# Performance work log

Hardware: AMD Instinct MI355X
Metric: run time of the kernel (lower is better)

The kernel has to match this reference:

```python
import jax, jax.numpy as jnp
import numpy as np

NUM_HEADS = 16
HIDDEN = 1024
HEAD_DIM = HIDDEN // NUM_HEADS


def setup_inputs() -> dict:
    key = jax.random.key(0)
    ks = jax.random.split(key, 9)
    B, S = 2, 2048
    s = 1.0 / np.sqrt(HIDDEN)
    return {
        "x": jax.random.normal(ks[0], (B, S, HIDDEN), dtype=jnp.float32),
        "Wq": jax.random.normal(ks[1], (HIDDEN, HIDDEN), dtype=jnp.float32) * s,
        "bq": jnp.zeros((HIDDEN,), dtype=jnp.float32),
        "Wk": jax.random.normal(ks[2], (HIDDEN, HIDDEN), dtype=jnp.float32) * s,
        "bk": jnp.zeros((HIDDEN,), dtype=jnp.float32),
        "Wv": jax.random.normal(ks[3], (HIDDEN, HIDDEN), dtype=jnp.float32) * s,
        "bv": jnp.zeros((HIDDEN,), dtype=jnp.float32),
        "Wo": jax.random.normal(ks[4], (HIDDEN, HIDDEN), dtype=jnp.float32) * s,
        "bo": jnp.zeros((HIDDEN,), dtype=jnp.float32),
    }


def reference(x, Wq, bq, Wk, bk, Wv, bv, Wo, bo):
    B, S, H = x.shape
    # project and split heads: [B, S, H] -> [B, nh, S, hd]
    def split_heads(t):
        return t.reshape(B, S, NUM_HEADS, HEAD_DIM).transpose(0, 2, 1, 3)

    q = split_heads(x @ Wq + bq)
    k = split_heads(x @ Wk + bk)
    v = split_heads(x @ Wv + bv)

    scores = jnp.einsum("bhqd,bhkd->bhqk", q, k) / jnp.sqrt(
        jnp.asarray(HEAD_DIM, dtype=x.dtype))
    probs = jax.nn.softmax(scores, axis=-1)
    # attn_drop_rate = 0.0 -> dropout is identity
    ctx = jnp.einsum("bhqk,bhkd->bhqd", probs, v)
    ctx = ctx.transpose(0, 2, 1, 3).reshape(B, S, H)
    out = ctx @ Wo + bo
    return out
```

## Files before the change

kernel.cpp:

```cpp
#include <hip/hip_runtime.h>

#define NHEADS 16
#define HDIM   64
#define SEQL   2048
#define HID    1024
#define NB     2
#define MT     4096

#define QSCALE 0.18033688011112042f
#define RESCALE_THR 6.0f

typedef float        f4_t   __attribute__((ext_vector_type(4)));
typedef float        f32x16 __attribute__((ext_vector_type(16)));
typedef unsigned int u32x4  __attribute__((ext_vector_type(4)));
typedef __bf16       bf16x8 __attribute__((ext_vector_type(8)));

typedef const __attribute__((address_space(1))) unsigned int* gas_ptr;
typedef __attribute__((address_space(3))) unsigned int*       las_ptr;

__device__ __forceinline__ void gload16(const void* g, void* l){
  __builtin_amdgcn_global_load_lds((gas_ptr)g, (las_ptr)l, 16, 0, 0);
}
__device__ __forceinline__ unsigned int pkbf(float a, float b){
  unsigned short lo = __builtin_bit_cast(unsigned short, (__bf16)a);
  unsigned short hi = __builtin_bit_cast(unsigned short, (__bf16)b);
  return (unsigned)lo | ((unsigned)hi << 16);
}
__device__ __forceinline__ unsigned short f2bf(float f){
  return __builtin_bit_cast(unsigned short, (__bf16)f);
}
__device__ __forceinline__ u32x4 ld16(const unsigned short* p){
  return *reinterpret_cast<const u32x4*>(p);
}
__device__ __forceinline__ f4_t mfma_bf16(u32x4 a, u32x4 b, f4_t c){
  return __builtin_amdgcn_mfma_f32_16x16x32_bf16(
      __builtin_bit_cast(bf16x8, a), __builtin_bit_cast(bf16x8, b), c, 0, 0, 0);
}
__device__ __forceinline__ f32x16 mfma32(u32x4 a, u32x4 b, f32x16 c){
  return __builtin_amdgcn_mfma_f32_32x32x16_bf16(
      __builtin_bit_cast(bf16x8, a), __builtin_bit_cast(bf16x8, b), c, 0, 0, 0);
}

#if __has_builtin(__builtin_amdgcn_permlane32_swap)
typedef unsigned int u32x2 __attribute__((ext_vector_type(2)));
__device__ __forceinline__ void plswap(unsigned int &a, unsigned int &b){
  u32x2 r = __builtin_amdgcn_permlane32_swap(a, b, false, false);
  a = r[0]; b = r[1];
}
#else
__device__ __forceinline__ void plswap(unsigned int &a, unsigned int &b){
  unsigned int as = (unsigned int)__shfl_xor((int)a, 32);
  unsigned int bs = (unsigned int)__shfl_xor((int)b, 32);
  bool hi = (threadIdx.x & 32) != 0;
  unsigned int na = hi ? bs : a;
  unsigned int nb = hi ? b  : as;
  a = na; b = nb;
}
#endif

__global__ __launch_bounds__(256) void xcast(const float* __restrict__ x,
                                             unsigned short* __restrict__ xb){
  int gid = blockIdx.x * 256 + threadIdx.x;
  float4 a = reinterpret_cast<const float4*>(x)[gid * 2];
  float4 b = reinterpret_cast<const float4*>(x)[gid * 2 + 1];
  u32x4 o;
  o[0] = pkbf(a.x, a.y);
  o[1] = pkbf(a.z, a.w);
  o[2] = pkbf(b.x, b.y);
  o[3] = pkbf(b.z, b.w);
  *reinterpret_cast<u32x4*>(&xb[gid * 8]) = o;
}

__global__ void prep_w(const float* __restrict__ Wq, const float* __restrict__ Wk,
                       const float* __restrict__ Wv, const float* __restrict__ Wo,
                       unsigned short* __restrict__ wqT, unsigned short* __restrict__ wkT,
                       unsigned short* __restrict__ wvT, unsigned short* __restrict__ woT){
  __shared__ float t[32][33];
  int z = blockIdx.z;
  const float* W = (z==0)?Wq:(z==1)?Wk:(z==2)?Wv:Wo;
  unsigned short* WT = (z==0)?wqT:(z==1)?wkT:(z==2)?wvT:woT;
  float sc = (z==0) ? QSCALE : 1.0f;
  int k0 = blockIdx.x*32, n0 = blockIdx.y*32;
  int tx = threadIdx.x, ty = threadIdx.y;
  #pragma unroll
  for (int ii=0; ii<4; ii++)
    t[ty+ii*8][tx] = W[(k0+ty+ii*8)*HID + n0+tx];
  __syncthreads();
  #pragma unroll
  for (int ii=0; ii<4; ii++)
    WT[(n0+ty+ii*8)*HID + k0+tx] = f2bf(t[tx][ty+ii*8] * sc);
}

__global__ __launch_bounds__(256) void qkv_gemm(
    const unsigned short* __restrict__ xb,
    const unsigned short* __restrict__ wqT, const unsigned short* __restrict__ wkT,
    const unsigned short* __restrict__ wvT,
    const float* __restrict__ bq, const float* __restrict__ bk, const float* __restrict__ bv,
    unsigned short* __restrict__ qo, unsigned short* __restrict__ ko,
    unsigned short* __restrict__ vto){
  __shared__ unsigned short As[128*32];
  __shared__ unsigned short Bs[128*32];
  const int z = blockIdx.z;
  const unsigned short* wT = (z==0)?wqT:(z==1)?wkT:wvT;
  const float* bias = (z==0)?bq:(z==1)?bk:bv;
  const float bscale = (z==0) ? QSCALE : 1.0f;
  const int m0 = blockIdx.x * 128;
  const int n0 = blockIdx.y * 128;
  const int tid = threadIdx.x;
  const int lane = tid & 63, w = tid >> 6;
  const int l15 = lane & 15, lg = lane >> 4;
  const int wr = (w >> 1) * 64, wc = (w & 1) * 64;
  const int srow = w*16 + (lane >> 2);
  const int skc  = (lane & 3) * 8;

  f4_t acc[4][4];
  f4_t z4 = {0.f, 0.f, 0.f, 0.f};
  #pragma unroll
  for (int i=0;i<4;i++)
    #pragma unroll
    for (int j=0;j<4;j++) acc[i][j] = z4;

  for (int kt = 0; kt < HID; kt += 32) {
    __syncthreads();
    #pragma unroll
    for (int c = 0; c < 2; c++) {
      int row = c*64 + srow;
      gload16(&xb[(m0+row)*HID + kt + skc], (char*)As + c*4096 + w*1024);
      gload16(&wT[(n0+row)*HID + kt + skc], (char*)Bs + c*4096 + w*1024);
    }
    __syncthreads();
    u32x4 a[4], b[4];
    #pragma unroll
    for (int i=0;i<4;i++) a[i] = ld16(&As[(wr + i*16 + l15)*32 + lg*8]);
    #pragma unroll
    for (int j=0;j<4;j++) b[j] = ld16(&Bs[(wc + j*16 + l15)*32 + lg*8]);
    #pragma unroll
    for (int i=0;i<4;i++)
      #pragma unroll
      for (int j=0;j<4;j++)
        acc[i][j] = mfma_bf16(a[i], b[j], acc[i][j]);
  }
  if (z == 2) {
    #pragma unroll
    for (int i=0;i<4;i++){
      int mrow = m0 + wr + i*16 + lg*4;
      int b_ = mrow >> 11, s = mrow & 2047;
      #pragma unroll
      for (int j=0;j<4;j++){
        int n = n0 + wc + j*16 + l15;
        float bs = bias[n];
        int h = n >> 6, d = n & 63;
        unsigned int lo = pkbf(acc[i][j][0]+bs, acc[i][j][1]+bs);
        unsigned int hi = pkbf(acc[i][j][2]+bs, acc[i][j][3]+bs);
        unsigned long long v8 = (unsigned long long)lo | ((unsigned long long)hi << 32);
        *reinterpret_cast<unsigned long long*>(
            vto + (((b_*NHEADS + h)*HDIM + d)*SEQL + s)) = v8;
      }
    }
  } else {
    unsigned short* outp = (z==0) ? qo : ko;
    #pragma unroll
    for (int i=0;i<4;i++){
      int mrow = m0 + wr + i*16 + lg*4;
      #pragma unroll
      for (int j=0;j<4;j++){
        int n = n0 + wc + j*16 + l15;
        float bs = bias[n] * bscale;
        int h = n >> 6, d = n & 63;
        #pragma unroll
        for (int r=0;r<4;r++){
          int m = mrow + r;
          int b_ = m >> 11, s = m & 2047;
          outp[(((b_*NHEADS + h)*SEQL) + s)*HDIM + d] = f2bf(acc[i][j][r] + bs);
        }
      }
    }
  }
}

__global__ __launch_bounds__(256) void flash(
    const unsigned short* __restrict__ q,
    const unsigned short* __restrict__ k,
    const unsigned short* __restrict__ vT,
    unsigned short* __restrict__ ctx){
  __shared__ unsigned short Ks[2][4096];
  __shared__ unsigned short Vs[2][4096];
  const int bh = blockIdx.y;
  const int b_ = bh >> 4, h = bh & 15;
  const int tid = threadIdx.x;
  const int w = tid >> 6, lane = tid & 63;
  const int l31 = lane & 31, hi = lane >> 5;
  const int q0 = blockIdx.x*128 + w*32;
  const unsigned short* qb = q + (bh*SEQL + q0)*HDIM;
  const unsigned short* kp = k + bh*SEQL*HDIM;
  const unsigned short* vp = vT + bh*HDIM*SEQL;

  const int sr = w*16 + (lane >> 3);
  const int scol = ((lane & 7) ^ (sr & 7)) * 8;
  const int ldst = w*2048;

  u32x4 qf[4];
  #pragma unroll
  for (int c=0;c<4;c++)
    qf[c] = ld16(&qb[l31*HDIM + c*16 + hi*8]);

  float mr = -1e30f, lsum = 0.f;
  f32x16 oacc[2];
  f32x16 z16 = {0.f,0.f,0.f,0.f,0.f,0.f,0.f,0.f,0.f,0.f,0.f,0.f,0.f,0.f,0.f,0.f};
  oacc[0] = z16; oacc[1] = z16;

  auto stage = [&](int buf, int kb){
    const unsigned short* gk = kp + (kb + sr)*HDIM + scol;
    gload16(gk,          (char*)Ks[buf] + ldst);
    gload16(gk + 8*HDIM, (char*)Ks[buf] + ldst + 1024);
    const unsigned short* gv = vp + sr*SEQL + kb + scol;
    gload16(gv,          (char*)Vs[buf] + ldst);
    gload16(gv + 8*SEQL, (char*)Vs[buf] + ldst + 1024);
  };

  int cur = 0;
  stage(0, 0);
  __syncthreads();

  const int rs = (l31 & 7) << 4;

  for (int kb = 0; kb < SEQL; kb += 64) {
    if (kb + 64 < SEQL) stage(cur^1, kb + 64);
    const char* kbase = (const char*)Ks[cur];
    const char* vbase = (const char*)Vs[cur];

    f32x16 sacc[2];
    __builtin_amdgcn_s_setprio(1);
    #pragma unroll
    for (int t=0;t<2;t++){
      const char* rowb = kbase + (t*32 + l31)*128;
      #pragma unroll
      for (int c=0;c<4;c++){
        u32x4 kf = *reinterpret_cast<const u32x4*>(rowb + ((c*32 + hi*16) ^ rs));
        sacc[t] = (c==0) ? mfma32(kf, qf[0], z16) : mfma32(kf, qf[c], sacc[t]);
      }
    }
    __builtin_amdgcn_s_setprio(0);

    float mx[16];
    #pragma unroll
    for (int r=0;r<16;r++) mx[r] = fmaxf(sacc[0][r], sacc[1][r]);
    #pragma unroll
    for (int r=0;r<8;r++) mx[r] = fmaxf(mx[r], mx[r+8]);
    #pragma unroll
    for (int r=0;r<4;r++) mx[r] = fmaxf(mx[r], mx[r+4]);
    float vm = fmaxf(fmaxf(mx[0], mx[1]), fmaxf(mx[2], mx[3]));
    vm = fmaxf(vm, __shfl_xor(vm, 32));
    if (!__all(vm - mr <= RESCALE_THR)) {
      float mnew = fmaxf(mr, vm);
      float scl = exp2f(mr - mnew);
      mr = mnew;
      lsum *= scl;
      oacc[0] *= scl;
      oacc[1] *= scl;
    }
    float sm[16];
    #pragma unroll
    for (int t=0;t<2;t++)
      #pragma unroll
      for (int r=0;r<16;r++) sacc[t][r] = exp2f(sacc[t][r] - mr);
    #pragma unroll
    for (int r=0;r<16;r++) sm[r] = sacc[0][r] + sacc[1][r];
    #pragma unroll
    for (int r=0;r<8;r++) sm[r] += sm[r+8];
    #pragma unroll
    for (int r=0;r<4;r++) sm[r] += sm[r+4];
    float ps = (sm[0] + sm[1]) + (sm[2] + sm[3]);
    ps += __shfl_xor(ps, 32);
    lsum += ps;

    u32x4 pa[4];
    #pragma unroll
    for (int t=0;t<2;t++)
      #pragma unroll
      for (int hf=0;hf<2;hf++){
        unsigned int c1 = pkbf(sacc[t][hf*8+0], sacc[t][hf*8+1]);
        unsigned int c2 = pkbf(sacc[t][hf*8+2], sacc[t][hf*8+3]);
        unsigned int c3 = pkbf(sacc[t][hf*8+4], sacc[t][hf*8+5]);
        unsigned int c4 = pkbf(sacc[t][hf*8+6], sacc[t][hf*8+7]);
        plswap(c1, c3);
        plswap(c2, c4);
        u32x4 f; f[0]=c1; f[1]=c2; f[2]=c3; f[3]=c4;
        pa[t*2+hf] = f;
      }

    __builtin_amdgcn_s_setprio(1);
    #pragma unroll
    for (int dt=0;dt<2;dt++){
      const char* rowb = vbase + (dt*32 + l31)*128;
      #pragma unroll
      for (int ks=0;ks<4;ks++){
        u32x4 vf = *reinterpret_cast<const u32x4*>(rowb + ((ks*32 + hi*16) ^ rs));
        oacc[dt] = mfma32(vf, pa[ks], oacc[dt]);
      }
    }
    __builtin_amdgcn_s_setprio(0);
    __syncthreads();
    cur ^= 1;
  }

  float inv = 1.0f / lsum;
  unsigned short* cb = ctx + (b_*SEQL + q0 + l31)*HID + h*HDIM;
  #pragma unroll
  for (int dt=0;dt<2;dt++){
    #pragma unroll
    for (int kq=0;kq<4;kq++){
      unsigned int lo = pkbf(oacc[dt][kq*4+0]*inv, oacc[dt][kq*4+1]*inv);
      unsigned int hi2 = pkbf(oacc[dt][kq*4+2]*inv, oacc[dt][kq*4+3]*inv);
      unsigned long long v8 = (unsigned long long)lo | ((unsigned long long)hi2 << 32);
      *reinterpret_cast<unsigned long long*>(cb + dt*32 + kq*8 + hi*4) = v8;
    }
  }
}

__global__ __launch_bounds__(256) void out_gemm(
    const unsigned short* __restrict__ cb,
    const unsigned short* __restrict__ woT,
    const float* __restrict__ bo,
    float* __restrict__ out){
  __shared__ unsigned short As[128*32];
  __shared__ unsigned short Bs[128*32];
  const int m0 = blockIdx.x * 128;
  const int n0 = blockIdx.y * 128;
  const int tid = threadIdx.x;
  const int lane = tid & 63, w = tid >> 6;
  const int l15 = lane & 15, lg = lane >> 4;
  const int wr = (w >> 1) * 64, wc = (w & 1) * 64;
  const int srow = w*16 + (lane >> 2);
  const int skc  = (lane & 3) * 8;

  f4_t acc[4][4];
  f4_t z4 = {0.f,0.f,0.f,0.f};
  #pragma unroll
  for (int i=0;i<4;i++)
    #pragma unroll
    for (int j=0;j<4;j++) acc[i][j] = z4;

  for (int kt = 0; kt < HID; kt += 32) {
    __syncthreads();
    #pragma unroll
    for (int c = 0; c < 2; c++) {
      int row = c*64 + srow;
      gload16(&cb[(m0+row)*HID + kt + skc],  (char*)As + c*4096 + w*1024);
      gload16(&woT[(n0+row)*HID + kt + skc], (char*)Bs + c*4096 + w*1024);
    }
    __syncthreads();
    u32x4 a[4], b[4];
    #pragma unroll
    for (int i=0;i<4;i++) a[i] = ld16(&As[(wr + i*16 + l15)*32 + lg*8]);
    #pragma unroll
    for (int j=0;j<4;j++) b[j] = ld16(&Bs[(wc + j*16 + l15)*32 + lg*8]);
    #pragma unroll
    for (int i=0;i<4;i++)
      #pragma unroll
      for (int j=0;j<4;j++)
        acc[i][j] = mfma_bf16(a[i], b[j], acc[i][j]);
  }
  #pragma unroll
  for (int i=0;i<4;i++){
    int mrow = m0 + wr + i*16 + lg*4;
    #pragma unroll
    for (int j=0;j<4;j++){
      int n = n0 + wc + j*16 + l15;
      float bs = bo[n];
      #pragma unroll
      for (int r=0;r<4;r++)
        out[(mrow + r)*HID + n] = acc[i][j][r] + bs;
    }
  }
}

extern "C" void kernel_launch(void* const* d_in, const int* in_sizes, int n_in,
                              void* d_out, int out_size, void* d_ws, size_t ws_size,
                              hipStream_t stream){
  const float* x  = (const float*)d_in[0];
  const float* Wq = (const float*)d_in[1];
  const float* bq = (const float*)d_in[2];
  const float* Wk = (const float*)d_in[3];
  const float* bk = (const float*)d_in[4];
  const float* Wv = (const float*)d_in[5];
  const float* bv = (const float*)d_in[6];
  const float* Wo = (const float*)d_in[7];
  const float* bo = (const float*)d_in[8];
  float* out = (float*)d_out;

  char* ws = (char*)d_ws;
  size_t off = 0;
  auto alloc = [&](size_t bytes) -> void* {
    void* p = ws + off;
    off += (bytes + 255) & ~(size_t)255;
    return p;
  };
  unsigned short* xb   = (unsigned short*)alloc((size_t)MT*HID*2);
  unsigned short* wqT  = (unsigned short*)alloc((size_t)HID*HID*2);
  unsigned short* wkT  = (unsigned short*)alloc((size_t)HID*HID*2);
  unsigned short* wvT  = (unsigned short*)alloc((size_t)HID*HID*2);
  unsigned short* woT  = (unsigned short*)alloc((size_t)HID*HID*2);
  unsigned short* q_ws = (unsigned short*)alloc((size_t)MT*HID*2);
  unsigned short* k_ws = (unsigned short*)alloc((size_t)MT*HID*2);
  unsigned short* vT_ws= (unsigned short*)alloc((size_t)MT*HID*2);
  unsigned short* c_ws = (unsigned short*)alloc((size_t)MT*HID*2);

  prep_w<<<dim3(32,32,4), dim3(32,8), 0, stream>>>(Wq,Wk,Wv,Wo, wqT,wkT,wvT,woT);
  xcast<<<dim3(2048), dim3(256), 0, stream>>>(x, xb);
  qkv_gemm<<<dim3(32,8,3), dim3(256), 0, stream>>>(xb, wqT,wkT,wvT, bq,bk,bv,
                                                   q_ws, k_ws, vT_ws);
  flash<<<dim3(16,32), dim3(256), 0, stream>>>(q_ws, k_ws, vT_ws, c_ws);
  out_gemm<<<dim3(32,8), dim3(256), 0, stream>>>(c_ws, woT, bo, out);
}
```

Baseline: 170.2 us.

## Split flash attention over key range and merge partials in a combine kernel

The flash kernel now splits the key sequence across blockIdx.z (flash-decoding style). Each split writes fp32 partial outputs plus running max and sum, and a new combine kernel rescales and merges them into the bf16 context. The aim is to raise the grid from 512 to 1024 blocks so the many CUs are better filled. The row sum is now computed with an MFMA against a ones vector, the row max uses a 3-input max tree, and launch bounds request 4 blocks per CU. The cost is extra fp32 partial traffic and an additional kernel launch, with a fallback to one split if the workspace is too small.

```diff
diff --git a/kernel.cpp b/kernel.cpp
--- a/kernel.cpp
+++ b/kernel.cpp
@@ -39,6 +39,9 @@
 __device__ __forceinline__ f32x16 mfma32(u32x4 a, u32x4 b, f32x16 c){
   return __builtin_amdgcn_mfma_f32_32x32x16_bf16(
       __builtin_bit_cast(bf16x8, a), __builtin_bit_cast(bf16x8, b), c, 0, 0, 0);
+}
+__device__ __forceinline__ float max3f(float a, float b, float c){
+  return fmaxf(fmaxf(a, b), c);
 }
 
 #if __has_builtin(__builtin_amdgcn_permlane32_swap)
@@ -178,15 +181,18 @@
   }
 }
 
-__global__ __launch_bounds__(256) void flash(
+__global__ __launch_bounds__(256, 4) void flash(
     const unsigned short* __restrict__ q,
     const unsigned short* __restrict__ k,
     const unsigned short* __restrict__ vT,
-    unsigned short* __restrict__ ctx){
+    float* __restrict__ po,
+    float* __restrict__ pml,
+    int kspan){
   __shared__ unsigned short Ks[2][4096];
   __shared__ unsigned short Vs[2][4096];
   const int bh = blockIdx.y;
-  const int b_ = bh >> 4, h = bh & 15;
+  const int z = blockIdx.z;
+  const int kb0 = z * kspan;
   const int tid = threadIdx.x;
   const int w = tid >> 6, lane = tid & 63;
   const int l31 = lane & 31, hi = lane >> 5;
@@ -204,10 +210,14 @@
   for (int c=0;c<4;c++)
     qf[c] = ld16(&qb[l31*HDIM + c*16 + hi*8]);
 
-  float mr = -1e30f, lsum = 0.f;
-  f32x16 oacc[2];
+  u32x4 ones;
+  ones[0] = 0x3F803F80u; ones[1] = 0x3F803F80u;
+  ones[2] = 0x3F803F80u; ones[3] = 0x3F803F80u;
+
+  float mr = -1e30f;
+  f32x16 oacc[2], lsacc;
   f32x16 z16 = {0.f,0.f,0.f,0.f,0.f,0.f,0.f,0.f,0.f,0.f,0.f,0.f,0.f,0.f,0.f,0.f};
-  oacc[0] = z16; oacc[1] = z16;
+  oacc[0] = z16; oacc[1] = z16; lsacc = z16;
 
   auto stage = [&](int buf, int kb){
     const unsigned short* gk = kp + (kb + sr)*HDIM + scol;
@@ -219,17 +229,18 @@
   };
 
   int cur = 0;
-  stage(0, 0);
+  stage(0, kb0);
   __syncthreads();
 
   const int rs = (l31 & 7) << 4;
 
-  for (int kb = 0; kb < SEQL; kb += 64) {
-    if (kb + 64 < SEQL) stage(cur^1, kb + 64);
+  for (int kb = kb0; kb < kb0 + kspan; kb += 64) {
+    if (kb + 64 < kb0 + kspan) stage(cur^1, kb + 64);
     const char* kbase = (const char*)Ks[cur];
     const char* vbase = (const char*)Vs[cur];
 
     f32x16 sacc[2];
+    sacc[0] = z16; sacc[1] = z16;
     __builtin_amdgcn_s_setprio(1);
     #pragma unroll
     for (int t=0;t<2;t++){
@@ -237,42 +248,36 @@
       #pragma unroll
       for (int c=0;c<4;c++){
         u32x4 kf = *reinterpret_cast<const u32x4*>(rowb + ((c*32 + hi*16) ^ rs));
-        sacc[t] = (c==0) ? mfma32(kf, qf[0], z16) : mfma32(kf, qf[c], sacc[t]);
+        sacc[t] = mfma32(kf, qf[c], sacc[t]);
       }
     }
     __builtin_amdgcn_s_setprio(0);
 
-    float mx[16];
-    #pragma unroll
-    for (int r=0;r<16;r++) mx[r] = fmaxf(sacc[0][r], sacc[1][r]);
-    #pragma unroll
-    for (int r=0;r<8;r++) mx[r] = fmaxf(mx[r], mx[r+8]);
-    #pragma unroll
-    for (int r=0;r<4;r++) mx[r] = fmaxf(mx[r], mx[r+4]);
-    float vm = fmaxf(fmaxf(mx[0], mx[1]), fmaxf(mx[2], mx[3]));
+    float v[32];
+    #pragma unroll
+    for (int r=0;r<16;r++){ v[r] = sacc[0][r]; v[16+r] = sacc[1][r]; }
+    float wv[11];
+    #pragma unroll
+    for (int g=0; g<10; g++) wv[g] = max3f(v[3*g], v[3*g+1], v[3*g+2]);
+    wv[10] = fmaxf(v[30], v[31]);
+    float u0 = max3f(wv[0], wv[1], wv[2]);
+    float u1 = max3f(wv[3], wv[4], wv[5]);
+    float u2 = max3f(wv[6], wv[7], wv[8]);
+    float u3 = fmaxf(wv[9], wv[10]);
+    float vm = fmaxf(fmaxf(u0, u1), fmaxf(u2, u3));
     vm = fmaxf(vm, __shfl_xor(vm, 32));
     if (!__all(vm - mr <= RESCALE_THR)) {
       float mnew = fmaxf(mr, vm);
       float scl = exp2f(mr - mnew);
       mr = mnew;
-      lsum *= scl;
+      lsacc *= scl;
       oacc[0] *= scl;
       oacc[1] *= scl;
     }
-    float sm[16];
     #pragma unroll
     for (int t=0;t<2;t++)
       #pragma unroll
       for (int r=0;r<16;r++) sacc[t][r] = exp2f(sacc[t][r] - mr);
-    #pragma unroll
-    for (int r=0;r<16;r++) sm[r] = sacc[0][r] + sacc[1][r];
-    #pragma unroll
-    for (int r=0;r<8;r++) sm[r] += sm[r+8];
-    #pragma unroll
-    for (int r=0;r<4;r++) sm[r] += sm[r+4];
-    float ps = (sm[0] + sm[1]) + (sm[2] + sm[3]);
-    ps += __shfl_xor(ps, 32);
-    lsum += ps;
 
     u32x4 pa[4];
     #pragma unroll
@@ -299,23 +304,63 @@
         oacc[dt] = mfma32(vf, pa[ks], oacc[dt]);
       }
     }
+    #pragma unroll
+    for (int ks=0;ks<4;ks++)
+      lsacc = mfma32(ones, pa[ks], lsacc);
     __builtin_amdgcn_s_setprio(0);
     __syncthreads();
     cur ^= 1;
   }
 
-  float inv = 1.0f / lsum;
-  unsigned short* cb = ctx + (b_*SEQL + q0 + l31)*HID + h*HDIM;
+  float lsum = lsacc[0];
+  const int pbase = ((z*NB*NHEADS + bh)*SEQL + q0 + l31)*HDIM;
   #pragma unroll
   for (int dt=0;dt<2;dt++){
     #pragma unroll
     for (int kq=0;kq<4;kq++){
-      unsigned int lo = pkbf(oacc[dt][kq*4+0]*inv, oacc[dt][kq*4+1]*inv);
-      unsigned int hi2 = pkbf(oacc[dt][kq*4+2]*inv, oacc[dt][kq*4+3]*inv);
-      unsigned long long v8 = (unsigned long long)lo | ((unsigned long long)hi2 << 32);
-      *reinterpret_cast<unsigned long long*>(cb + dt*32 + kq*8 + hi*4) = v8;
-    }
-  }
+      float4 o4;
+      o4.x = oacc[dt][kq*4+0]; o4.y = oacc[dt][kq*4+1];
+      o4.z = oacc[dt][kq*4+2]; o4.w = oacc[dt][kq*4+3];
+      *reinterpret_cast<float4*>(po + pbase + dt*32 + kq*8 + hi*4) = o4;
+    }
+  }
+  if (hi == 0) {
+    float2 ml; ml.x = mr; ml.y = lsum;
+    *reinterpret_cast<float2*>(pml + ((z*NB*NHEADS + bh)*SEQL + q0 + l31)*2) = ml;
+  }
+}
+
+__global__ __launch_bounds__(256) void combine(
+    const float* __restrict__ po, const float* __restrict__ pml,
+    unsigned short* __restrict__ ctx, int nsplit){
+  int i = blockIdx.x*256 + threadIdx.x;
+  int dq = i & 15;
+  int rsi = i >> 4;
+  int bh = rsi >> 11, s = rsi & 2047;
+  int b_ = bh >> 4, h = bh & 15;
+  float2 ml0 = reinterpret_cast<const float2*>(pml)[rsi];
+  float4 o0 = reinterpret_cast<const float4*>(po)[rsi*16 + dq];
+  float L; float4 acc;
+  if (nsplit == 2) {
+    float2 ml1 = reinterpret_cast<const float2*>(pml)[rsi + NB*NHEADS*SEQL];
+    float4 o1 = reinterpret_cast<const float4*>(po)[rsi*16 + dq + NB*NHEADS*SEQL*16];
+    float M = fmaxf(ml0.x, ml1.x);
+    float w0 = exp2f(ml0.x - M), w1 = exp2f(ml1.x - M);
+    L = w0*ml0.y + w1*ml1.y;
+    acc.x = w0*o0.x + w1*o1.x;
+    acc.y = w0*o0.y + w1*o1.y;
+    acc.z = w0*o0.z + w1*o1.z;
+    acc.w = w0*o0.w + w1*o1.w;
+  } else {
+    L = ml0.y;
+    acc = o0;
+  }
+  float inv = 1.0f / L;
+  unsigned int lo = pkbf(acc.x*inv, acc.y*inv);
+  unsigned int hv = pkbf(acc.z*inv, acc.w*inv);
+  unsigned long long v8 = (unsigned long long)lo | ((unsigned long long)hv << 32);
+  *reinterpret_cast<unsigned long long*>(
+      ctx + (b_*SEQL + s)*HID + h*HDIM + dq*4) = v8;
 }
 
 __global__ __launch_bounds__(256) void out_gemm(
@@ -405,11 +450,24 @@
   unsigned short* k_ws = (unsigned short*)alloc((size_t)MT*HID*2);
   unsigned short* vT_ws= (unsigned short*)alloc((size_t)MT*HID*2);
   unsigned short* c_ws = (unsigned short*)alloc((size_t)MT*HID*2);
+  size_t off1 = off;
+  float* po  = (float*)alloc((size_t)2*MT*HID*4);
+  float* pml = (float*)alloc((size_t)2*MT*NHEADS*2*4);
+  size_t off2 = off;
+
+  int nsplit = (ws_size >= off2) ? 2 : 1;
+  if (nsplit == 1) {
+    po  = (float*)((char*)ws + off1);
+    pml = (float*)((char*)po + (size_t)MT*HID*4 + 256);
+  }
+  int kspan = SEQL / nsplit;
 
   prep_w<<<dim3(32,32,4), dim3(32,8), 0, stream>>>(Wq,Wk,Wv,Wo, wqT,wkT,wvT,woT);
   xcast<<<dim3(2048), dim3(256), 0, stream>>>(x, xb);
   qkv_gemm<<<dim3(32,8,3), dim3(256), 0, stream>>>(xb, wqT,wkT,wvT, bq,bk,bv,
                                                    q_ws, k_ws, vT_ws);
-  flash<<<dim3(16,32), dim3(256), 0, stream>>>(q_ws, k_ws, vT_ws, c_ws);
+  flash<<<dim3(16,32,nsplit), dim3(256), 0, stream>>>(q_ws, k_ws, vT_ws,
+                                                      po, pml, kspan);
+  combine<<<dim3(MT*HID/4/256), dim3(256), 0, stream>>>(po, pml, c_ws, nsplit);
   out_gemm<<<dim3(32,8), dim3(256), 0, stream>>>(c_ws, woT, bo, out);
 }
```

New measurement: 161.3 us. 5.2% less time.
